# Kernel optimization log

Measured on AMD Instinct MI355X. Metric: run time of the kernel, lower is better.

## Reference

```python
import jax, jax.numpy as jnp
import numpy as np

N, F_IN, E, H, C, B = 50000, 128, 800000, 64, 10, 512


def gcn_conv(x, W, b, src, dst, n):
    # PyG GCNConv: h = xW; add self-loops; norm = d^-1/2[src]*d^-1/2[dst]; scatter-add; + bias
    h = x @ W
    deg = jax.ops.segment_sum(jnp.ones(src.shape[0], h.dtype), dst, num_segments=n) + 1.0  # +1 self-loop
    dinv = jax.lax.rsqrt(deg)
    msg = h[src] * (dinv[src] * dinv[dst])[:, None]            # [E, H] gather + scale
    out = jax.ops.segment_sum(msg, dst, num_segments=n)        # scatter-add over targets
    out = out + h * (dinv * dinv)[:, None]                      # self-loop term (norm = 1/deg)
    return out + b


def setup_inputs() -> dict:
    key = jax.random.key(0)
    ks = jax.random.split(key, 12)
    x = jax.random.normal(ks[0], (N, F_IN), dtype=jnp.float32)
    edge_index = jax.random.randint(ks[1], (2, E), 0, N)
    batch = jnp.sort(jax.random.randint(ks[2], (N,), 0, B))
    def glorot(k, fan_in, fan_out):
        s = np.sqrt(6.0 / (fan_in + fan_out)).astype(np.float32)
        return jax.random.uniform(k, (fan_in, fan_out), jnp.float32, -s, s)
    return {
        "x": x, "edge_index": edge_index, "batch": batch,
        "W1": glorot(ks[3], F_IN, H), "b1": jnp.zeros((H,), jnp.float32),
        "W2": glorot(ks[4], H, H),    "b2": jnp.zeros((H,), jnp.float32),
        "W3": glorot(ks[5], H, H),    "b3": jnp.zeros((H,), jnp.float32),
        "Wl": glorot(ks[6], H, C),    "bl": jnp.zeros((C,), jnp.float32),
    }


def reference(x, edge_index, batch, W1, b1, W2, b2, W3, b3, Wl, bl):
    src, dst = edge_index[0], edge_index[1]
    n = x.shape[0]
    h = jax.nn.relu(gcn_conv(x, W1, b1, src, dst, n))
    h = jax.nn.relu(gcn_conv(h, W2, b2, src, dst, n))
    h = gcn_conv(h, W3, b3, src, dst, n)
    # global mean pool over graphs
    sums = jax.ops.segment_sum(h, batch, num_segments=B)
    cnts = jax.ops.segment_sum(jnp.ones((n,), h.dtype), batch, num_segments=B)
    pooled = sums / jnp.maximum(cnts, 1.0)[:, None]
    # dropout is identity in eval mode
    return pooled @ Wl + bl
```

## Files before the change

kernel.cpp:

```cpp
#include <hip/hip_runtime.h>

#define NBSHIFT 8
#define MAXB    5120
#define CHUNK   4096
#define TPB     256

__device__ inline unsigned short f2bf(float f) {
    unsigned u = __builtin_bit_cast(unsigned, f);
    unsigned r = u + 0x7FFFu + ((u >> 16) & 1u);
    return (unsigned short)(r >> 16);
}
__device__ inline float bflo(unsigned u) { return __builtin_bit_cast(float, u << 16); }
__device__ inline float bfhi(unsigned u) { return __builtin_bit_cast(float, u & 0xFFFF0000u); }

__global__ void k_init(int* __restrict__ bcur, int NB) {
    int t = threadIdx.x;
    if (t < NB) bcur[t] = 0;
}

__global__ __launch_bounds__(TPB) void k_bin_seg(const int* __restrict__ src,
                                                 const int* __restrict__ dst,
                                                 int* __restrict__ bcur,
                                                 unsigned* __restrict__ pairbuf,
                                                 const int* __restrict__ batch,
                                                 int* __restrict__ segs,
                                                 int* __restrict__ sege,
                                                 int E, int N, int B, int NB,
                                                 int nbChunk) {
    __shared__ int sdst[CHUNK];
    __shared__ int lcnt[256];
    __shared__ int lbase[256];
    int t = threadIdx.x;
    if ((int)blockIdx.x < nbChunk) {
        int e0 = blockIdx.x * CHUNK;
        int n = min(e0 + CHUNK, E) - e0;
        lcnt[t] = 0;
        __syncthreads();
        for (int i = t; i < n; i += TPB) {
            int d = dst[e0 + i];
            sdst[i] = d;
            atomicAdd(&lcnt[d >> NBSHIFT], 1);
        }
        __syncthreads();
        if (t < NB) {
            int c = lcnt[t];
            lbase[t] = c ? atomicAdd(&bcur[t], c) : 0;
            lcnt[t] = 0;
        }
        __syncthreads();
        for (int i = t; i < n; i += TPB) {
            int d = sdst[i];
            int b = d >> NBSHIFT;
            int pos = lbase[b] + atomicAdd(&lcnt[b], 1);
            pairbuf[(size_t)b * MAXB + pos] =
                ((unsigned)(d & 255) << 24) | (unsigned)src[e0 + i];
        }
    } else {
        int g = ((int)blockIdx.x - nbChunk) * TPB + t;
        if (g < B) {
            int lo = 0, hi = N;
            while (lo < hi) { int m = (lo + hi) >> 1; if (batch[m] < g) lo = m + 1; else hi = m; }
            int s = lo;
            lo = s; hi = N;
            while (lo < hi) { int m = (lo + hi) >> 1; if (batch[m] < g + 1) lo = m + 1; else hi = m; }
            segs[g] = s;
            sege[g] = lo;
        }
    }
}

template <int KHALVES>
__device__ void gemm_tile(const float* __restrict__ in, const float* __restrict__ W,
                          const float* __restrict__ sc, unsigned short* __restrict__ outb,
                          int tile, int N, float* sf) {
    float* sX = sf;
    float* sW = sf + 4096;
    const int K = KHALVES * 64;
    int t = threadIdx.x, w = t >> 6, l = t & 63;
    int node0 = tile * 64;
    int fg = l & 15, ngl = w * 4 + (l >> 4);
    float4 a0 = make_float4(0.f, 0.f, 0.f, 0.f), a1 = a0, a2 = a0, a3 = a0;

    for (int h = 0; h < KHALVES; ++h) {
        __syncthreads();
        for (int i = t; i < 64 * 16; i += TPB)
            ((float4*)sW)[i] = ((const float4*)(W + h * 64 * 64))[i];
        {
            int node = node0 + l;
            bool ok = node < N;
            const float* rp = in + (size_t)node * K + h * 64;
            for (int k0 = w * 16; k0 < w * 16 + 16; k0 += 4) {
                float4 v = ok ? *(const float4*)(rp + k0) : make_float4(0.f, 0.f, 0.f, 0.f);
                sX[(k0 + 0) * 64 + l] = v.x;
                sX[(k0 + 1) * 64 + l] = v.y;
                sX[(k0 + 2) * 64 + l] = v.z;
                sX[(k0 + 3) * 64 + l] = v.w;
            }
        }
        __syncthreads();
#pragma unroll 8
        for (int k = 0; k < 64; ++k) {
            float4 xv = *(const float4*)(sX + k * 64 + ngl * 4);
            float4 wv = *(const float4*)(sW + k * 64 + fg * 4);
            a0.x += xv.x * wv.x; a0.y += xv.x * wv.y; a0.z += xv.x * wv.z; a0.w += xv.x * wv.w;
            a1.x += xv.y * wv.x; a1.y += xv.y * wv.y; a1.z += xv.y * wv.z; a1.w += xv.y * wv.w;
            a2.x += xv.z * wv.x; a2.y += xv.z * wv.y; a2.z += xv.z * wv.z; a2.w += xv.z * wv.w;
            a3.x += xv.w * wv.x; a3.y += xv.w * wv.y; a3.z += xv.w * wv.z; a3.w += xv.w * wv.w;
        }
    }
    int nbase = node0 + ngl * 4;
    float4 accs[4] = {a0, a1, a2, a3};
#pragma unroll
    for (int i = 0; i < 4; ++i) {
        int n = nbase + i;
        if (n < N) {
            float s = sc ? sc[n] : 1.0f;
            float4 o = accs[i];
            ushort4 ob;
            ob.x = f2bf(o.x * s); ob.y = f2bf(o.y * s);
            ob.z = f2bf(o.z * s); ob.w = f2bf(o.w * s);
            *(ushort4*)(outb + (size_t)n * 64 + fg * 4) = ob;
        }
    }
}

__global__ __launch_bounds__(TPB) void k_build_gemm1(const unsigned* __restrict__ pairbuf,
                                                     const int* __restrict__ bcur,
                                                     int* __restrict__ pofs,
                                                     float* __restrict__ dinv,
                                                     int* __restrict__ ssrc,
                                                     const float* __restrict__ x,
                                                     const float* __restrict__ W1,
                                                     unsigned short* __restrict__ hsb,
                                                     int N, int NB) {
    __shared__ __align__(16) float sf[8192];
    int* si = (int*)sf;
    int t = threadIdx.x;
    int bid = blockIdx.x;
    if (bid < NB) {
        int* hcnt = si;
        int* sd   = si + 256;
        int* hcur = si + 512;
        size_t s0 = (size_t)bid * MAXB;
        int cb = bcur[bid];
        hcnt[t] = 0;
        __syncthreads();
        for (int i = t; i < cb; i += TPB)
            atomicAdd(&hcnt[pairbuf[s0 + i] >> 24], 1);
        __syncthreads();
        int c = hcnt[t];
        sd[t] = c;
        __syncthreads();
        int sum = c;
        for (int d = 1; d < 256; d <<= 1) {
            int a = (t >= d) ? sd[t - d] : 0;
            __syncthreads();
            sum += a; sd[t] = sum;
            __syncthreads();
        }
        int excl = sum - c;
        int node = (bid << NBSHIFT) + t;
        if (node < N) {
            pofs[node] = (excl << 8) | c;
            dinv[node] = rsqrtf((float)c + 1.0f);
        }
        hcur[t] = excl;
        __syncthreads();
        for (int i = t; i < cb; i += TPB) {
            unsigned p = pairbuf[s0 + i];
            int pos = atomicAdd(&hcur[p >> 24], 1);
            ssrc[s0 + pos] = (int)(p & 0x00FFFFFFu);
        }
    } else {
        gemm_tile<2>(x, W1, nullptr, hsb, bid - NB, N, sf);
    }
}

__global__ __launch_bounds__(TPB) void k_gemm64(const float* __restrict__ in,
                                                const float* __restrict__ W,
                                                const float* __restrict__ dinv,
                                                unsigned short* __restrict__ outb,
                                                int N) {
    __shared__ __align__(16) float sf[8192];
    gemm_tile<1>(in, W, dinv, outb, blockIdx.x, N, sf);
}

template <bool EDGEDINV, bool RELU>
__global__ __launch_bounds__(TPB) void k_agg(const unsigned short* __restrict__ hs,
                                             const int* __restrict__ ssrc,
                                             const int* __restrict__ pofs,
                                             const float* __restrict__ dinv,
                                             const float* __restrict__ bias,
                                             float* __restrict__ outp, int N) {
    int t = threadIdx.x;
    int wave = t >> 6, lane = t & 63;
    int g = lane >> 4, fl = lane & 15;
    int v = blockIdx.x * 4 + wave;
    if (v >= N) return;
    int pk = pofs[v];
    size_t start = (size_t)(v >> NBSHIFT) * MAXB + (pk >> 8);
    int cnt = pk & 255;
    float dv = dinv[v];
    float4 acc = make_float4(0.f, 0.f, 0.f, 0.f);
#define BF_ACCS(p, s)                                                          \
    do {                                                                       \
        acc.x += bflo((p).x) * (s); acc.y += bfhi((p).x) * (s);                \
        acc.z += bflo((p).y) * (s); acc.w += bfhi((p).y) * (s);                \
    } while (0)
    if (g == 0) {
        uint2 p = *(const uint2*)(hs + (size_t)v * 64 + fl * 4);
        float sc = EDGEDINV ? dv : 1.0f;
        BF_ACCS(p, sc);
    }
    int j = 0, cnt16 = cnt & ~15;
    for (; j < cnt16; j += 16) {
        int s0 = ssrc[start + j + g];
        int s1 = ssrc[start + j + 4 + g];
        int s2 = ssrc[start + j + 8 + g];
        int s3 = ssrc[start + j + 12 + g];
        float d0 = 1.f, d1 = 1.f, d2 = 1.f, d3 = 1.f;
        if (EDGEDINV) { d0 = dinv[s0]; d1 = dinv[s1]; d2 = dinv[s2]; d3 = dinv[s3]; }
        uint2 h0 = *(const uint2*)(hs + (size_t)s0 * 64 + fl * 4);
        uint2 h1 = *(const uint2*)(hs + (size_t)s1 * 64 + fl * 4);
        uint2 h2 = *(const uint2*)(hs + (size_t)s2 * 64 + fl * 4);
        uint2 h3 = *(const uint2*)(hs + (size_t)s3 * 64 + fl * 4);
        BF_ACCS(h0, d0); BF_ACCS(h1, d1); BF_ACCS(h2, d2); BF_ACCS(h3, d3);
    }
    int cnt4 = cnt & ~3;
    for (; j < cnt4; j += 4) {
        int s = ssrc[start + j + g];
        float d = EDGEDINV ? dinv[s] : 1.f;
        uint2 h = *(const uint2*)(hs + (size_t)s * 64 + fl * 4);
        BF_ACCS(h, d);
    }
    int rem = cnt - cnt4;
    if (g < rem) {
        int s = ssrc[start + cnt4 + g];
        float d = EDGEDINV ? dinv[s] : 1.f;
        uint2 h = *(const uint2*)(hs + (size_t)s * 64 + fl * 4);
        BF_ACCS(h, d);
    }
#undef BF_ACCS
    acc.x += __shfl_xor(acc.x, 16); acc.y += __shfl_xor(acc.y, 16);
    acc.z += __shfl_xor(acc.z, 16); acc.w += __shfl_xor(acc.w, 16);
    acc.x += __shfl_xor(acc.x, 32); acc.y += __shfl_xor(acc.y, 32);
    acc.z += __shfl_xor(acc.z, 32); acc.w += __shfl_xor(acc.w, 32);
    if (g == 0) {
        float4 bv = *(const float4*)(bias + fl * 4);
        float4 o;
        o.x = acc.x * dv + bv.x; o.y = acc.y * dv + bv.y;
        o.z = acc.z * dv + bv.z; o.w = acc.w * dv + bv.w;
        if (RELU) {
            o.x = fmaxf(o.x, 0.f); o.y = fmaxf(o.y, 0.f);
            o.z = fmaxf(o.z, 0.f); o.w = fmaxf(o.w, 0.f);
        }
        *(float4*)(outp + (size_t)v * 64 + fl * 4) = o;
    }
}

__global__ __launch_bounds__(64) void k_pool_classify(const float* __restrict__ h,
                                                      const int* __restrict__ ss,
                                                      const int* __restrict__ se,
                                                      const float* __restrict__ Wl,
                                                      const float* __restrict__ bl,
                                                      float* __restrict__ out, int C) {
    int b = blockIdx.x;
    int lane = threadIdx.x;
    int g = lane >> 4, fl = lane & 15;
    int s = ss[b], e = se[b];
    float4 acc = make_float4(0.f, 0.f, 0.f, 0.f);
#pragma unroll 2
    for (int v = s + g; v < e; v += 4) {
        float4 hv = *(const float4*)(h + (size_t)v * 64 + fl * 4);
        acc.x += hv.x; acc.y += hv.y; acc.z += hv.z; acc.w += hv.w;
    }
    acc.x += __shfl_xor(acc.x, 16); acc.y += __shfl_xor(acc.y, 16);
    acc.z += __shfl_xor(acc.z, 16); acc.w += __shfl_xor(acc.w, 16);
    acc.x += __shfl_xor(acc.x, 32); acc.y += __shfl_xor(acc.y, 32);
    acc.z += __shfl_xor(acc.z, 32); acc.w += __shfl_xor(acc.w, 32);
    if (g == 0) {
        int cnt = e - s;
        if (cnt < 1) cnt = 1;
        float inv = 1.0f / (float)cnt;
        float4 p;
        p.x = acc.x * inv; p.y = acc.y * inv; p.z = acc.z * inv; p.w = acc.w * inv;
        int f0 = fl * 4;
        for (int c = 0; c < C; ++c) {
            float tt = p.x * Wl[(f0 + 0) * C + c] + p.y * Wl[(f0 + 1) * C + c]
                     + p.z * Wl[(f0 + 2) * C + c] + p.w * Wl[(f0 + 3) * C + c];
            tt += __shfl_xor(tt, 1); tt += __shfl_xor(tt, 2);
            tt += __shfl_xor(tt, 4); tt += __shfl_xor(tt, 8);
            if (fl == 0) out[b * C + c] = tt + bl[c];
        }
    }
}


extern "C" void kernel_launch(void* const* d_in, const int* in_sizes, int n_in,
                              void* d_out, int out_size, void* d_ws, size_t ws_size,
                              hipStream_t stream) {
    const float* x    = (const float*)d_in[0];
    const int*   ei   = (const int*)d_in[1];
    const int*   batch= (const int*)d_in[2];
    const float* W1   = (const float*)d_in[3];
    const float* b1   = (const float*)d_in[4];
    const float* W2   = (const float*)d_in[5];
    const float* b2   = (const float*)d_in[6];
    const float* W3   = (const float*)d_in[7];
    const float* b3   = (const float*)d_in[8];
    const float* Wl   = (const float*)d_in[9];
    const float* bl   = (const float*)d_in[10];
    float* out = (float*)d_out;

    const int N = in_sizes[2];
    const int E = in_sizes[1] / 2;
    const int C = 10;
    const int B = out_size / C;
    const int NB = (N + (1 << NBSHIFT) - 1) >> NBSHIFT;
    const int nbChunk = (E + CHUNK - 1) / CHUNK;
    const int nbSeg = (B + TPB - 1) / TPB;
    const int ntiles = (N + 63) / 64;

    char* ws = (char*)d_ws;
    auto alloc = [&](size_t bytes) {
        char* p = ws;
        ws += (bytes + 255) & ~(size_t)255;
        return p;
    };
    int*   bcur = (int*)alloc((size_t)NB * 4);
    int*   segs = (int*)alloc((size_t)B * 4);
    int*   sege = (int*)alloc((size_t)B * 4);
    int*   pofs = (int*)alloc((size_t)N * 4);
    float* dinv = (float*)alloc((size_t)N * 4);
    int*   ssrc = (int*)alloc((size_t)NB * MAXB * 4);
    unsigned short* hsb = (unsigned short*)alloc((size_t)N * 64 * 2);
    float* act  = (float*)alloc((size_t)N * 64 * 4);
    unsigned* pairbuf = (unsigned*)act;

    const int* src = ei;
    const int* dst = ei + E;

    int gAgg = (N + 3) / 4;

    k_init<<<1, TPB, 0, stream>>>(bcur, NB);
    k_bin_seg<<<nbChunk + nbSeg, TPB, 0, stream>>>(src, dst, bcur, pairbuf,
                                                   batch, segs, sege, E, N, B, NB, nbChunk);
    k_build_gemm1<<<NB + ntiles, TPB, 0, stream>>>(pairbuf, bcur, pofs, dinv, ssrc,
                                                   x, W1, hsb, N, NB);
    k_agg<true, true><<<gAgg, TPB, 0, stream>>>(hsb, ssrc, pofs, dinv, b1, act, N);
    k_gemm64<<<ntiles, TPB, 0, stream>>>(act, W2, dinv, hsb, N);
    k_agg<false, true><<<gAgg, TPB, 0, stream>>>(hsb, ssrc, pofs, dinv, b2, act, N);
    k_gemm64<<<ntiles, TPB, 0, stream>>>(act, W3, dinv, hsb, N);
    k_agg<false, false><<<gAgg, TPB, 0, stream>>>(hsb, ssrc, pofs, dinv, b3, act, N);
    k_pool_classify<<<B, 64, 0, stream>>>(act, segs, sege, Wl, bl, out, C);
}
```

Before: 165.1 us.

## Fuse neighbor aggregation with next-layer 64x64 GEMM in persistent kernel

Layers 1 and 2 no longer aggregate into an fp32 buffer and then run a separate GEMM. Each wave now aggregates one node's row, broadcasts it with shuffles, multiplies it by the next weight matrix held in shared memory, and writes the bf16 result scaled by dinv. This removes the fp32 activation write and re-read plus two launches, and ping-pongs between two bf16 buffers. In exchange it uses a per-row shuffle-based matvec instead of a tiled GEMM, and a fixed grid-stride launch of 2048 blocks.

Measured after the change: 197.2 us. 1.19x slower.

```diff
diff --git a/kernel.cpp b/kernel.cpp
--- a/kernel.cpp
+++ b/kernel.cpp
@@ -4,6 +4,7 @@
 #define MAXB    5120
 #define CHUNK   4096
 #define TPB     256
+#define FUSEBLK 2048
 
 __device__ inline unsigned short f2bf(float f) {
     unsigned u = __builtin_bit_cast(unsigned, f);
@@ -176,31 +177,17 @@
     }
 }
 
-__global__ __launch_bounds__(TPB) void k_gemm64(const float* __restrict__ in,
-                                                const float* __restrict__ W,
-                                                const float* __restrict__ dinv,
-                                                unsigned short* __restrict__ outb,
-                                                int N) {
-    __shared__ __align__(16) float sf[8192];
-    gemm_tile<1>(in, W, dinv, outb, blockIdx.x, N, sf);
-}
-
 template <bool EDGEDINV, bool RELU>
-__global__ __launch_bounds__(TPB) void k_agg(const unsigned short* __restrict__ hs,
-                                             const int* __restrict__ ssrc,
-                                             const int* __restrict__ pofs,
-                                             const float* __restrict__ dinv,
-                                             const float* __restrict__ bias,
-                                             float* __restrict__ outp, int N) {
-    int t = threadIdx.x;
-    int wave = t >> 6, lane = t & 63;
-    int g = lane >> 4, fl = lane & 15;
-    int v = blockIdx.x * 4 + wave;
-    if (v >= N) return;
+__device__ float4 agg_row(const unsigned short* __restrict__ hs,
+                          const int* __restrict__ ssrc, const int* __restrict__ pofs,
+                          const float* __restrict__ dinv, const float* __restrict__ bias,
+                          int v, float& dv_out) {
+    int lane = threadIdx.x & 63, g = lane >> 4, fl = lane & 15;
     int pk = pofs[v];
     size_t start = (size_t)(v >> NBSHIFT) * MAXB + (pk >> 8);
     int cnt = pk & 255;
     float dv = dinv[v];
+    dv_out = dv;
     float4 acc = make_float4(0.f, 0.f, 0.f, 0.f);
 #define BF_ACCS(p, s)                                                          \
     do {                                                                       \
@@ -245,17 +232,67 @@
     acc.z += __shfl_xor(acc.z, 16); acc.w += __shfl_xor(acc.w, 16);
     acc.x += __shfl_xor(acc.x, 32); acc.y += __shfl_xor(acc.y, 32);
     acc.z += __shfl_xor(acc.z, 32); acc.w += __shfl_xor(acc.w, 32);
-    if (g == 0) {
-        float4 bv = *(const float4*)(bias + fl * 4);
-        float4 o;
-        o.x = acc.x * dv + bv.x; o.y = acc.y * dv + bv.y;
-        o.z = acc.z * dv + bv.z; o.w = acc.w * dv + bv.w;
-        if (RELU) {
-            o.x = fmaxf(o.x, 0.f); o.y = fmaxf(o.y, 0.f);
-            o.z = fmaxf(o.z, 0.f); o.w = fmaxf(o.w, 0.f);
-        }
+    float4 bv = *(const float4*)(bias + fl * 4);
+    float4 o;
+    o.x = acc.x * dv + bv.x; o.y = acc.y * dv + bv.y;
+    o.z = acc.z * dv + bv.z; o.w = acc.w * dv + bv.w;
+    if (RELU) {
+        o.x = fmaxf(o.x, 0.f); o.y = fmaxf(o.y, 0.f);
+        o.z = fmaxf(o.z, 0.f); o.w = fmaxf(o.w, 0.f);
+    }
+    return o;
+}
+
+template <bool EDGEDINV>
+__global__ __launch_bounds__(TPB) void k_agg_gemm(const unsigned short* __restrict__ hs,
+                                                  const int* __restrict__ ssrc,
+                                                  const int* __restrict__ pofs,
+                                                  const float* __restrict__ dinv,
+                                                  const float* __restrict__ bias,
+                                                  const float* __restrict__ W,
+                                                  unsigned short* __restrict__ outb,
+                                                  int N) {
+    __shared__ float sW[64 * 64];
+    int t = threadIdx.x;
+    for (int i = t; i < 64 * 16; i += TPB)
+        ((float4*)sW)[i] = ((const float4*)W)[i];
+    __syncthreads();
+    int wave = t >> 6, lane = t & 63;
+    for (int v = blockIdx.x * 4 + wave; v < N; v += FUSEBLK * 4) {
+        float dv;
+        float4 row = agg_row<EDGEDINV, true>(hs, ssrc, pofs, dinv, bias, v, dv);
+        float o = 0.f;
+#pragma unroll
+        for (int i = 0; i < 16; ++i) {
+            float4 r4;
+            r4.x = __shfl(row.x, i);
+            r4.y = __shfl(row.y, i);
+            r4.z = __shfl(row.z, i);
+            r4.w = __shfl(row.w, i);
+            o += r4.x * sW[(i * 4 + 0) * 64 + lane]
+               + r4.y * sW[(i * 4 + 1) * 64 + lane]
+               + r4.z * sW[(i * 4 + 2) * 64 + lane]
+               + r4.w * sW[(i * 4 + 3) * 64 + lane];
+        }
+        outb[(size_t)v * 64 + lane] = f2bf(o * dv);
+    }
+}
+
+__global__ __launch_bounds__(TPB) void k_agg3(const unsigned short* __restrict__ hs,
+                                              const int* __restrict__ ssrc,
+                                              const int* __restrict__ pofs,
+                                              const float* __restrict__ dinv,
+                                              const float* __restrict__ bias,
+                                              float* __restrict__ outp, int N) {
+    int t = threadIdx.x;
+    int wave = t >> 6, lane = t & 63;
+    int g = lane >> 4, fl = lane & 15;
+    int v = blockIdx.x * 4 + wave;
+    if (v >= N) return;
+    float dv;
+    float4 o = agg_row<false, false>(hs, ssrc, pofs, dinv, bias, v, dv);
+    if (g == 0)
         *(float4*)(outp + (size_t)v * 64 + fl * 4) = o;
-    }
 }
 
 __global__ __launch_bounds__(64) void k_pool_classify(const float* __restrict__ h,
@@ -333,7 +370,8 @@
     int*   pofs = (int*)alloc((size_t)N * 4);
     float* dinv = (float*)alloc((size_t)N * 4);
     int*   ssrc = (int*)alloc((size_t)NB * MAXB * 4);
-    unsigned short* hsb = (unsigned short*)alloc((size_t)N * 64 * 2);
+    unsigned short* hsb  = (unsigned short*)alloc((size_t)N * 64 * 2);
+    unsigned short* hsb2 = (unsigned short*)alloc((size_t)N * 64 * 2);
     float* act  = (float*)alloc((size_t)N * 64 * 4);
     unsigned* pairbuf = (unsigned*)act;
 
@@ -347,10 +385,8 @@
                                                    batch, segs, sege, E, N, B, NB, nbChunk);
     k_build_gemm1<<<NB + ntiles, TPB, 0, stream>>>(pairbuf, bcur, pofs, dinv, ssrc,
                                                    x, W1, hsb, N, NB);
-    k_agg<true, true><<<gAgg, TPB, 0, stream>>>(hsb, ssrc, pofs, dinv, b1, act, N);
-    k_gemm64<<<ntiles, TPB, 0, stream>>>(act, W2, dinv, hsb, N);
-    k_agg<false, true><<<gAgg, TPB, 0, stream>>>(hsb, ssrc, pofs, dinv, b2, act, N);
-    k_gemm64<<<ntiles, TPB, 0, stream>>>(act, W3, dinv, hsb, N);
-    k_agg<false, false><<<gAgg, TPB, 0, stream>>>(hsb, ssrc, pofs, dinv, b3, act, N);
+    k_agg_gemm<true><<<FUSEBLK, TPB, 0, stream>>>(hsb, ssrc, pofs, dinv, b1, W2, hsb2, N);
+    k_agg_gemm<false><<<FUSEBLK, TPB, 0, stream>>>(hsb2, ssrc, pofs, dinv, b2, W3, hsb, N);
+    k_agg3<<<gAgg, TPB, 0, stream>>>(hsb, ssrc, pofs, dinv, b3, act, N);
     k_pool_classify<<<B, 64, 0, stream>>>(act, segs, sege, Wl, bl, out, C);
 }
```
